# Kernel optimization log

Measured on AMD Instinct MI355X. Metric: run time of the kernel, lower is better.

## Reference

```python
import jax, jax.numpy as jnp
import numpy as np


def _apply_1q_batched(state, gate, q):
    # state: (B,2,2,2,2) complex; gate: (B,2,2) complex; acts on qubit q
    state = jnp.moveaxis(state, q + 1, -1)
    state = jnp.einsum('bij,b...j->b...i', gate, state)
    return jnp.moveaxis(state, -1, q + 1)


def _apply_cnot(state, c, t):
    # flip target bit where control bit == 1
    s0, s1 = jnp.split(state, 2, axis=c + 1)
    s1 = jnp.flip(s1, axis=t + 1)
    return jnp.concatenate([s0, s1], axis=c + 1)


def _quantum_features(angles, params):
    # angles: (B,4) RY rotation angles; params: (4,) RZ angles
    B = angles.shape[0]
    state = jnp.zeros((B, 16), jnp.complex64).at[:, 0].set(1.0).reshape(B, 2, 2, 2, 2)
    # RY(x_i) on each wire (batched angle per sample)
    for q in range(4):
        th = 0.5 * angles[:, q]
        c, s = jnp.cos(th), jnp.sin(th)
        gate = jnp.stack([jnp.stack([c, -s], -1), jnp.stack([s, c], -1)], -2).astype(jnp.complex64)
        state = _apply_1q_batched(state, gate, q)
    # RZ(params[i]) on wire i followed by CNOT(i, (i+1)%4), interleaved as in source
    pc = params.astype(jnp.complex64)
    for q in range(4):
        ph = jnp.exp(jnp.array([-0.5j, 0.5j], jnp.complex64) * pc[q])
        shp = [1, 1, 1, 1, 1]
        shp[q + 1] = 2
        state = state * ph.reshape(shp)
        state = _apply_cnot(state, q, (q + 1) % 4)
    probs = state.real ** 2 + state.imag ** 2  # (B,2,2,2,2)
    feats = []
    for q in range(4):
        axes = tuple(a for a in range(1, 5) if a != q + 1)
        p = probs.sum(axes)  # (B,2)
        feats.append(p[:, 0] - p[:, 1])  # <Z_q>
    return jnp.stack(feats, -1)  # (B,4)


def _deconv2x2(x, w, b):
    # PyTorch ConvTranspose2d with kernel=stride=2, padding=0 (non-overlapping)
    # x: (B,Ci,H,W), w: (Ci,Co,2,2), b: (Co,)
    B, Ci, H, W = x.shape
    Co = w.shape[1]
    y = jnp.einsum('bchw,codk->bohdwk', x, w).reshape(B, Co, 2 * H, 2 * W)
    return y + b[None, :, None, None]


def setup_inputs() -> dict:
    key = jax.random.key(0)
    ks = jax.random.split(key, 10)
    B = 16384
    return {
        'x': jax.random.uniform(ks[0], (B, 1, 28, 28), jnp.float32),
        'var_params': jax.random.normal(ks[1], (4,), jnp.float32),
        'w_lat': jax.random.normal(ks[2], (224, 4), jnp.float32) * 0.3,
        'b_lat': jax.random.normal(ks[3], (224,), jnp.float32) * 0.05,
        'w_fc': jax.random.normal(ks[4], (392, 224), jnp.float32) * 0.05,
        'b_fc': jax.random.normal(ks[5], (392,), jnp.float32) * 0.05,
        'w_d1': jax.random.normal(ks[6], (8, 4, 2, 2), jnp.float32) * 0.2,
        'b_d1': jax.random.normal(ks[7], (4,), jnp.float32) * 0.05,
        'w_d2': jax.random.normal(ks[8], (4, 1, 2, 2), jnp.float32) * 0.2,
        'b_d2': jax.random.normal(ks[9], (1,), jnp.float32) * 0.05,
    }


def reference(x, var_params, w_lat, b_lat, w_fc, b_fc, w_d1, b_d1, w_d2, b_d2):
    # quadrant means -> 4 angles per sample
    quad = jnp.stack([
        x[:, 0, :14, :14].mean((1, 2)),
        x[:, 0, :14, 14:].mean((1, 2)),
        x[:, 0, 14:, :14].mean((1, 2)),
        x[:, 0, 14:, 14:].mean((1, 2)),
    ], axis=1)  # (B,4)
    qf = _quantum_features(quad, var_params)  # (B,4)
    latent = jax.nn.relu(qf @ w_lat.T + b_lat)  # (B,224)
    h = jax.nn.relu(latent @ w_fc.T + b_fc)  # (B,392)
    h = h.reshape(-1, 8, 7, 7)
    h = jax.nn.relu(_deconv2x2(h, w_d1, b_d1))  # (B,4,14,14)
    out = jax.nn.sigmoid(_deconv2x2(h, w_d2, b_d2))  # (B,1,28,28)
    return out
```

## Files before the change

kernel.cpp:

```cpp
#include <hip/hip_runtime.h>
#include <math.h>

#define G 16
#define HS2 400
#define LSTR 232

typedef __attribute__((ext_vector_type(8))) __bf16 bf16x8;
typedef __attribute__((ext_vector_type(4))) float f32x4;
typedef __attribute__((ext_vector_type(2))) float f32x2;

__global__ void wconv_kernel(const float* __restrict__ w_fc, __bf16* __restrict__ wb) {
  int tile = blockIdx.x;
  int kt   = blockIdx.y;
  int lane = threadIdx.x;
  int n  = tile * 16 + (lane & 15);
  int k0 = kt * 32 + (lane >> 4) * 8;
  bf16x8 v;
  if (n < 392) {
    const float* src = w_fc + (size_t)n * 224 + k0;
    float4 f0 = *(const float4*)(src);
    float4 f1 = *(const float4*)(src + 4);
    v[0] = (__bf16)f0.x; v[1] = (__bf16)f0.y; v[2] = (__bf16)f0.z; v[3] = (__bf16)f0.w;
    v[4] = (__bf16)f1.x; v[5] = (__bf16)f1.y; v[6] = (__bf16)f1.z; v[7] = (__bf16)f1.w;
  } else {
    #pragma unroll
    for (int j = 0; j < 8; ++j) v[j] = (__bf16)0.f;
  }
  *(bf16x8*)(wb + ((size_t)(tile * 7 + kt) * 64 + lane) * 8) = v;
}

__global__ __launch_bounds__(512, 8) void fused_kernel(
    const float* __restrict__ x, const float* __restrict__ params,
    const __bf16* __restrict__ wb,
    const float* __restrict__ w_lat, const float* __restrict__ b_lat,
    const float* __restrict__ b_fc,
    const float* __restrict__ w_d1, const float* __restrict__ b_d1,
    const float* __restrict__ w_d2, const float* __restrict__ b_d2,
    float* __restrict__ out, int B)
{
  __shared__ __align__(16) __bf16 latb[G * LSTR];
  __shared__ __align__(16) __bf16 hbuf[G * HS2];
  __shared__ __align__(16) float qfs[G * 4];
  __shared__ float wd1[128];
  __shared__ float wd2[16];
  __shared__ float bd1[4];
  const int t = threadIdx.x;
  const int wv = t >> 6;
  const int lane = t & 63;
  const int s0g = blockIdx.x * G;
  if (s0g >= B) return;

  if (t < 128) wd1[t] = w_d1[t];
  else if (t < 144) wd2[t - 128] = w_d2[t - 128];
  else if (t < 148) bd1[t - 144] = b_d1[t - 144];

  {
    const float* xb = x + (size_t)(s0g + wv * 2) * 784;
    f32x4 vb[2][4];
    #pragma unroll
    for (int smp = 0; smp < 2; ++smp)
      #pragma unroll
      for (int it = 0; it < 4; ++it) {
        int i4 = lane + it * 64;
        if (i4 < 196)
          vb[smp][it] = __builtin_nontemporal_load((const f32x4*)(xb + smp * 784 + i4 * 4));
        else
          vb[smp][it] = (f32x4){0.f, 0.f, 0.f, 0.f};
      }
    float acc[2][4];
    #pragma unroll
    for (int i = 0; i < 2; ++i)
      #pragma unroll
      for (int q = 0; q < 4; ++q) acc[i][q] = 0.f;
    #pragma unroll
    for (int it = 0; it < 4; ++it) {
      int i4 = lane + it * 64;
      int base = i4 * 4;
      int r = base / 28;
      int cb = base - r * 28;
      float bt = (r >= 14) ? 1.f : 0.f;
      float tp = 1.f - bt;
      float w0[4], w1[4], w2[4], w3[4];
      #pragma unroll
      for (int e = 0; e < 4; ++e) {
        float lf = ((cb + e) < 14) ? 1.f : 0.f;
        float rf = 1.f - lf;
        w0[e] = tp * lf; w1[e] = tp * rf; w2[e] = bt * lf; w3[e] = bt * rf;
      }
      #pragma unroll
      for (int smp = 0; smp < 2; ++smp) {
        f32x4 v = vb[smp][it];
        #pragma unroll
        for (int e = 0; e < 4; ++e) {
          acc[smp][0] = fmaf(v[e], w0[e], acc[smp][0]);
          acc[smp][1] = fmaf(v[e], w1[e], acc[smp][1]);
          acc[smp][2] = fmaf(v[e], w2[e], acc[smp][2]);
          acc[smp][3] = fmaf(v[e], w3[e], acc[smp][3]);
        }
      }
    }
    #pragma unroll
    for (int smp = 0; smp < 2; ++smp)
      #pragma unroll
      for (int q = 0; q < 4; ++q)
        #pragma unroll
        for (int o = 32; o > 0; o >>= 1)
          acc[smp][q] += __shfl_down(acc[smp][q], o, 64);
    if (lane == 0) {
      const float inv = 1.f / 196.f;
      #pragma unroll
      for (int smp = 0; smp < 2; ++smp) {
        float4 o;
        o.x = acc[smp][0] * inv; o.y = acc[smp][1] * inv;
        o.z = acc[smp][2] * inv; o.w = acc[smp][3] * inv;
        *(float4*)(qfs + (wv * 2 + smp) * 4) = o;
      }
    }
  }

  {
    const int sub = lane >> 4;
    const int i   = lane & 15;
    const int s   = wv * 2 + (sub & 1);
    float4 mn = *(const float4*)(qfs + s * 4);
    float c_[4], s_[4];
    c_[0] = __cosf(0.5f * mn.x); s_[0] = __sinf(0.5f * mn.x);
    c_[1] = __cosf(0.5f * mn.y); s_[1] = __sinf(0.5f * mn.y);
    c_[2] = __cosf(0.5f * mn.z); s_[2] = __sinf(0.5f * mn.z);
    c_[3] = __cosf(0.5f * mn.w); s_[3] = __sinf(0.5f * mn.w);
    float re = (((i >> 3) & 1) ? s_[0] : c_[0]) * (((i >> 2) & 1) ? s_[1] : c_[1])
             * (((i >> 1) & 1) ? s_[2] : c_[2]) * ((i & 1) ? s_[3] : c_[3]);
    float im = 0.f;
    #pragma unroll
    for (int q = 0; q < 4; ++q) {
      float hp = 0.5f * params[q];
      float sp = __sinf(hp), cp = __cosf(hp);
      int qb = 3 - q;
      float sg = ((i >> qb) & 1) ? sp : -sp;
      float r0 = re, i0 = im;
      re = r0 * cp - i0 * sg;
      im = r0 * sg + i0 * cp;
      int cm = 1 << qb;
      int tm = 1 << (3 - ((q + 1) & 3));
      int srcI = (i & cm) ? (i ^ tm) : i;
      int srcLane = (lane & ~15) | srcI;
      re = __shfl(re, srcLane, 64);
      im = __shfl(im, srcLane, 64);
    }
    float p = re * re + im * im;
    float z[4];
    #pragma unroll
    for (int q = 0; q < 4; ++q) {
      int qb = 3 - q;
      float v = ((i >> qb) & 1) ? -p : p;
      v += __shfl_xor(v, 1, 16);
      v += __shfl_xor(v, 2, 16);
      v += __shfl_xor(v, 4, 16);
      v += __shfl_xor(v, 8, 16);
      z[q] = v;
    }
    if (sub < 2 && i < 4) {
      float zv = (i == 0) ? z[0] : (i == 1) ? z[1] : (i == 2) ? z[2] : z[3];
      qfs[s * 4 + i] = zv;
    }
  }

  #pragma unroll
  for (int sl = 0; sl < 2; ++sl) {
    int s = wv * 2 + sl;
    float4 q4 = *(const float4*)(qfs + s * 4);
    for (int j = lane; j < 224; j += 64) {
      float4 w = *(const float4*)(w_lat + j * 4);
      float a = b_lat[j];
      a = fmaf(q4.x, w.x, a);
      a = fmaf(q4.y, w.y, a);
      a = fmaf(q4.z, w.z, a);
      a = fmaf(q4.w, w.w, a);
      latb[s * LSTR + j] = (__bf16)fmaxf(a, 0.f);
    }
  }
  __syncthreads();

  {
    const int m = lane & 15;
    const int kq = lane >> 4;
    const __bf16* arow = latb + m * LSTR + kq * 8;
    for (int tile = wv; tile < 25; tile += 8) {
      f32x4 acc = {0.f, 0.f, 0.f, 0.f};
      const bf16x8* bp = (const bf16x8*)(wb + ((size_t)(tile * 7) * 64 + lane) * 8);
      #pragma unroll
      for (int kt = 0; kt < 7; ++kt) {
        bf16x8 a = *(const bf16x8*)(arow + kt * 32);
        bf16x8 b = bp[kt * 64];
        acc = __builtin_amdgcn_mfma_f32_16x16x32_bf16(a, b, acc, 0, 0, 0);
      }
      int j = tile * 16 + m;
      if (j < 392) {
        float bf = b_fc[j];
        #pragma unroll
        for (int r = 0; r < 4; ++r)
          hbuf[(kq * 4 + r) * HS2 + j] = (__bf16)fmaxf(acc[r] + bf, 0.f);
      }
    }
  }
  __syncthreads();

  const float bd2v = b_d2[0];
  for (int v = t; v < G * 196; v += 512) {
    int s = v / 196;
    int p = v - s * 196;
    int Y = p / 14;
    int X = p - Y * 14;
    int y = Y >> 1, ey = Y & 1, xx = X >> 1, ex = X & 1;
    const __bf16* hs = hbuf + s * HS2 + y * 7 + xx;
    float hv[8];
    #pragma unroll
    for (int ci = 0; ci < 8; ++ci) hv[ci] = (float)hs[ci * 49];
    float o1[4];
    #pragma unroll
    for (int co = 0; co < 4; ++co) {
      float a = bd1[co];
      #pragma unroll
      for (int ci = 0; ci < 8; ++ci)
        a = fmaf(hv[ci], wd1[ci * 16 + co * 4 + ey * 2 + ex], a);
      o1[co] = fmaxf(a, 0.f);
    }
    size_t basep = (size_t)(s0g + s) * 784;
    #pragma unroll
    for (int dy = 0; dy < 2; ++dy) {
      float v0 = bd2v, v1 = bd2v;
      #pragma unroll
      for (int co = 0; co < 4; ++co) {
        v0 = fmaf(o1[co], wd2[co * 4 + dy * 2 + 0], v0);
        v1 = fmaf(o1[co], wd2[co * 4 + dy * 2 + 1], v1);
      }
      f32x2 o;
      o[0] = 1.f / (1.f + __expf(-v0));
      o[1] = 1.f / (1.f + __expf(-v1));
      __builtin_nontemporal_store(o, (f32x2*)(out + basep + (size_t)(2 * Y + dy) * 28 + 2 * X));
    }
  }
}

extern "C" void kernel_launch(void* const* d_in, const int* in_sizes, int n_in,
                              void* d_out, int out_size, void* d_ws, size_t ws_size,
                              hipStream_t stream) {
  const float* x          = (const float*)d_in[0];
  const float* var_params = (const float*)d_in[1];
  const float* w_lat      = (const float*)d_in[2];
  const float* b_lat      = (const float*)d_in[3];
  const float* w_fc       = (const float*)d_in[4];
  const float* b_fc       = (const float*)d_in[5];
  const float* w_d1       = (const float*)d_in[6];
  const float* b_d1       = (const float*)d_in[7];
  const float* w_d2       = (const float*)d_in[8];
  const float* b_d2       = (const float*)d_in[9];
  float* out = (float*)d_out;

  __bf16* wb = (__bf16*)d_ws;

  int B = in_sizes[0] / 784;
  wconv_kernel<<<dim3(25, 7), 64, 0, stream>>>(w_fc, wb);
  fused_kernel<<<(B + G - 1) / G, 512, 0, stream>>>(
      x, var_params, wb, w_lat, b_lat, b_fc, w_d1, b_d1, w_d2, b_d2, out, B);
}
```

Measured before the change: 135.6 us.

## Process two sample groups per block with prefetch, restructure deconv epilogue layout

Each block now handles two groups of 16 samples and prefetches the second group's input while the first group's quantum and GEMM stages run. The hidden buffer is relaid out channel-interleaved so each deconv thread reads one 16-byte vector and produces a 4x4 output patch written as four float4 nontemporal stores, replacing scattered 8-byte stores. The RZ cos/sin values are computed once in the weight-conversion kernel, and launch bounds are relaxed to 4 blocks per SM. The risks are higher register pressure from the prefetched vectors and half as many blocks for spreading work across the GPU.

```diff
diff --git a/kernel.cpp b/kernel.cpp
--- a/kernel.cpp
+++ b/kernel.cpp
@@ -2,14 +2,14 @@
 #include <math.h>
 
 #define G 16
-#define HS2 400
+#define HS 408
 #define LSTR 232
 
 typedef __attribute__((ext_vector_type(8))) __bf16 bf16x8;
 typedef __attribute__((ext_vector_type(4))) float f32x4;
-typedef __attribute__((ext_vector_type(2))) float f32x2;
-
-__global__ void wconv_kernel(const float* __restrict__ w_fc, __bf16* __restrict__ wb) {
+
+__global__ void wconv_kernel(const float* __restrict__ w_fc, const float* __restrict__ params,
+                             __bf16* __restrict__ wb, float* __restrict__ aux) {
   int tile = blockIdx.x;
   int kt   = blockIdx.y;
   int lane = threadIdx.x;
@@ -27,11 +27,31 @@
     for (int j = 0; j < 8; ++j) v[j] = (__bf16)0.f;
   }
   *(bf16x8*)(wb + ((size_t)(tile * 7 + kt) * 64 + lane) * 8) = v;
+  if (tile == 0 && kt == 0 && lane < 4) {
+    float hp = 0.5f * params[lane];
+    aux[2 * lane]     = __cosf(hp);
+    aux[2 * lane + 1] = __sinf(hp);
+  }
 }
 
-__global__ __launch_bounds__(512, 8) void fused_kernel(
-    const float* __restrict__ x, const float* __restrict__ params,
-    const __bf16* __restrict__ wb,
+__device__ __forceinline__ void load_vb(f32x4 (&dst)[2][4], const float* __restrict__ x,
+                                        int sbase, int wv, int lane) {
+  const float* xb = x + (size_t)(sbase + wv * 2) * 784;
+  #pragma unroll
+  for (int smp = 0; smp < 2; ++smp)
+    #pragma unroll
+    for (int it = 0; it < 4; ++it) {
+      int i4 = lane + it * 64;
+      if (i4 < 196)
+        dst[smp][it] = __builtin_nontemporal_load((const f32x4*)(xb + smp * 784 + i4 * 4));
+      else
+        dst[smp][it] = (f32x4){0.f, 0.f, 0.f, 0.f};
+    }
+}
+
+__global__ __launch_bounds__(512, 4) void fused_kernel(
+    const float* __restrict__ x, const __bf16* __restrict__ wb,
+    const float* __restrict__ aux,
     const float* __restrict__ w_lat, const float* __restrict__ b_lat,
     const float* __restrict__ b_fc,
     const float* __restrict__ w_d1, const float* __restrict__ b_d1,
@@ -39,206 +59,225 @@
     float* __restrict__ out, int B)
 {
   __shared__ __align__(16) __bf16 latb[G * LSTR];
-  __shared__ __align__(16) __bf16 hbuf[G * HS2];
+  __shared__ __align__(16) __bf16 hbuf[G * HS];
   __shared__ __align__(16) float qfs[G * 4];
-  __shared__ float wd1[128];
-  __shared__ float wd2[16];
-  __shared__ float bd1[4];
+  __shared__ __align__(16) float wd1[128];
+  __shared__ __align__(16) float wd2[16];
+  __shared__ __align__(16) float bd1[4];
   const int t = threadIdx.x;
   const int wv = t >> 6;
   const int lane = t & 63;
-  const int s0g = blockIdx.x * G;
-  if (s0g >= B) return;
+  int s0 = blockIdx.x * (2 * G);
+  if (s0 >= B) return;
 
   if (t < 128) wd1[t] = w_d1[t];
   else if (t < 144) wd2[t - 128] = w_d2[t - 128];
   else if (t < 148) bd1[t - 144] = b_d1[t - 144];
 
-  {
-    const float* xb = x + (size_t)(s0g + wv * 2) * 784;
-    f32x4 vb[2][4];
-    #pragma unroll
-    for (int smp = 0; smp < 2; ++smp)
+  f32x4 vb[2][4];
+  load_vb(vb, x, s0, wv, lane);
+
+  #pragma unroll
+  for (int g = 0; g < 2; ++g) {
+    {
+      float acc[2][4];
+      #pragma unroll
+      for (int i = 0; i < 2; ++i)
+        #pragma unroll
+        for (int q = 0; q < 4; ++q) acc[i][q] = 0.f;
       #pragma unroll
       for (int it = 0; it < 4; ++it) {
         int i4 = lane + it * 64;
-        if (i4 < 196)
-          vb[smp][it] = __builtin_nontemporal_load((const f32x4*)(xb + smp * 784 + i4 * 4));
-        else
-          vb[smp][it] = (f32x4){0.f, 0.f, 0.f, 0.f};
-      }
-    float acc[2][4];
+        int base = i4 * 4;
+        int r = base / 28;
+        int cb = base - r * 28;
+        float bt = (r >= 14) ? 1.f : 0.f;
+        float tp = 1.f - bt;
+        float w0[4], w1[4], w2[4], w3[4];
+        #pragma unroll
+        for (int e = 0; e < 4; ++e) {
+          float lf = ((cb + e) < 14) ? 1.f : 0.f;
+          float rf = 1.f - lf;
+          w0[e] = tp * lf; w1[e] = tp * rf; w2[e] = bt * lf; w3[e] = bt * rf;
+        }
+        #pragma unroll
+        for (int smp = 0; smp < 2; ++smp) {
+          f32x4 v = vb[smp][it];
+          #pragma unroll
+          for (int e = 0; e < 4; ++e) {
+            acc[smp][0] = fmaf(v[e], w0[e], acc[smp][0]);
+            acc[smp][1] = fmaf(v[e], w1[e], acc[smp][1]);
+            acc[smp][2] = fmaf(v[e], w2[e], acc[smp][2]);
+            acc[smp][3] = fmaf(v[e], w3[e], acc[smp][3]);
+          }
+        }
+      }
+      #pragma unroll
+      for (int smp = 0; smp < 2; ++smp)
+        #pragma unroll
+        for (int q = 0; q < 4; ++q)
+          #pragma unroll
+          for (int o = 32; o > 0; o >>= 1)
+            acc[smp][q] += __shfl_down(acc[smp][q], o, 64);
+      if (lane == 0) {
+        const float inv = 1.f / 196.f;
+        #pragma unroll
+        for (int smp = 0; smp < 2; ++smp) {
+          float4 o;
+          o.x = acc[smp][0] * inv; o.y = acc[smp][1] * inv;
+          o.z = acc[smp][2] * inv; o.w = acc[smp][3] * inv;
+          *(float4*)(qfs + (wv * 2 + smp) * 4) = o;
+        }
+      }
+    }
+
+    if (g == 0 && s0 + G < B) load_vb(vb, x, s0 + G, wv, lane);
+
+    {
+      const int sub = lane >> 4;
+      const int i   = lane & 15;
+      const int s   = wv * 2 + (sub & 1);
+      float4 mn = *(const float4*)(qfs + s * 4);
+      float c_[4], s_[4];
+      c_[0] = __cosf(0.5f * mn.x); s_[0] = __sinf(0.5f * mn.x);
+      c_[1] = __cosf(0.5f * mn.y); s_[1] = __sinf(0.5f * mn.y);
+      c_[2] = __cosf(0.5f * mn.z); s_[2] = __sinf(0.5f * mn.z);
+      c_[3] = __cosf(0.5f * mn.w); s_[3] = __sinf(0.5f * mn.w);
+      float re = (((i >> 3) & 1) ? s_[0] : c_[0]) * (((i >> 2) & 1) ? s_[1] : c_[1])
+               * (((i >> 1) & 1) ? s_[2] : c_[2]) * ((i & 1) ? s_[3] : c_[3]);
+      float im = 0.f;
+      #pragma unroll
+      for (int q = 0; q < 4; ++q) {
+        float cp = aux[2 * q], sp = aux[2 * q + 1];
+        int qb = 3 - q;
+        float sg = ((i >> qb) & 1) ? sp : -sp;
+        float r0 = re, i0 = im;
+        re = r0 * cp - i0 * sg;
+        im = r0 * sg + i0 * cp;
+        int cm = 1 << qb;
+        int tm = 1 << (3 - ((q + 1) & 3));
+        int srcI = (i & cm) ? (i ^ tm) : i;
+        int srcLane = (lane & ~15) | srcI;
+        re = __shfl(re, srcLane, 64);
+        im = __shfl(im, srcLane, 64);
+      }
+      float p = re * re + im * im;
+      float z[4];
+      #pragma unroll
+      for (int q = 0; q < 4; ++q) {
+        int qb = 3 - q;
+        float v = ((i >> qb) & 1) ? -p : p;
+        v += __shfl_xor(v, 1, 16);
+        v += __shfl_xor(v, 2, 16);
+        v += __shfl_xor(v, 4, 16);
+        v += __shfl_xor(v, 8, 16);
+        z[q] = v;
+      }
+      if (sub < 2 && i < 4) {
+        float zv = (i == 0) ? z[0] : (i == 1) ? z[1] : (i == 2) ? z[2] : z[3];
+        qfs[s * 4 + i] = zv;
+      }
+    }
+
     #pragma unroll
-    for (int i = 0; i < 2; ++i)
-      #pragma unroll
-      for (int q = 0; q < 4; ++q) acc[i][q] = 0.f;
-    #pragma unroll
-    for (int it = 0; it < 4; ++it) {
-      int i4 = lane + it * 64;
-      int base = i4 * 4;
-      int r = base / 28;
-      int cb = base - r * 28;
-      float bt = (r >= 14) ? 1.f : 0.f;
-      float tp = 1.f - bt;
-      float w0[4], w1[4], w2[4], w3[4];
-      #pragma unroll
-      for (int e = 0; e < 4; ++e) {
-        float lf = ((cb + e) < 14) ? 1.f : 0.f;
-        float rf = 1.f - lf;
-        w0[e] = tp * lf; w1[e] = tp * rf; w2[e] = bt * lf; w3[e] = bt * rf;
-      }
-      #pragma unroll
-      for (int smp = 0; smp < 2; ++smp) {
-        f32x4 v = vb[smp][it];
-        #pragma unroll
-        for (int e = 0; e < 4; ++e) {
-          acc[smp][0] = fmaf(v[e], w0[e], acc[smp][0]);
-          acc[smp][1] = fmaf(v[e], w1[e], acc[smp][1]);
-          acc[smp][2] = fmaf(v[e], w2[e], acc[smp][2]);
-          acc[smp][3] = fmaf(v[e], w3[e], acc[smp][3]);
-        }
-      }
-    }
-    #pragma unroll
-    for (int smp = 0; smp < 2; ++smp)
-      #pragma unroll
-      for (int q = 0; q < 4; ++q)
-        #pragma unroll
-        for (int o = 32; o > 0; o >>= 1)
-          acc[smp][q] += __shfl_down(acc[smp][q], o, 64);
-    if (lane == 0) {
-      const float inv = 1.f / 196.f;
-      #pragma unroll
-      for (int smp = 0; smp < 2; ++smp) {
-        float4 o;
-        o.x = acc[smp][0] * inv; o.y = acc[smp][1] * inv;
-        o.z = acc[smp][2] * inv; o.w = acc[smp][3] * inv;
-        *(float4*)(qfs + (wv * 2 + smp) * 4) = o;
-      }
-    }
-  }
-
-  {
-    const int sub = lane >> 4;
-    const int i   = lane & 15;
-    const int s   = wv * 2 + (sub & 1);
-    float4 mn = *(const float4*)(qfs + s * 4);
-    float c_[4], s_[4];
-    c_[0] = __cosf(0.5f * mn.x); s_[0] = __sinf(0.5f * mn.x);
-    c_[1] = __cosf(0.5f * mn.y); s_[1] = __sinf(0.5f * mn.y);
-    c_[2] = __cosf(0.5f * mn.z); s_[2] = __sinf(0.5f * mn.z);
-    c_[3] = __cosf(0.5f * mn.w); s_[3] = __sinf(0.5f * mn.w);
-    float re = (((i >> 3) & 1) ? s_[0] : c_[0]) * (((i >> 2) & 1) ? s_[1] : c_[1])
-             * (((i >> 1) & 1) ? s_[2] : c_[2]) * ((i & 1) ? s_[3] : c_[3]);
-    float im = 0.f;
-    #pragma unroll
-    for (int q = 0; q < 4; ++q) {
-      float hp = 0.5f * params[q];
-      float sp = __sinf(hp), cp = __cosf(hp);
-      int qb = 3 - q;
-      float sg = ((i >> qb) & 1) ? sp : -sp;
-      float r0 = re, i0 = im;
-      re = r0 * cp - i0 * sg;
-      im = r0 * sg + i0 * cp;
-      int cm = 1 << qb;
-      int tm = 1 << (3 - ((q + 1) & 3));
-      int srcI = (i & cm) ? (i ^ tm) : i;
-      int srcLane = (lane & ~15) | srcI;
-      re = __shfl(re, srcLane, 64);
-      im = __shfl(im, srcLane, 64);
-    }
-    float p = re * re + im * im;
-    float z[4];
-    #pragma unroll
-    for (int q = 0; q < 4; ++q) {
-      int qb = 3 - q;
-      float v = ((i >> qb) & 1) ? -p : p;
-      v += __shfl_xor(v, 1, 16);
-      v += __shfl_xor(v, 2, 16);
-      v += __shfl_xor(v, 4, 16);
-      v += __shfl_xor(v, 8, 16);
-      z[q] = v;
-    }
-    if (sub < 2 && i < 4) {
-      float zv = (i == 0) ? z[0] : (i == 1) ? z[1] : (i == 2) ? z[2] : z[3];
-      qfs[s * 4 + i] = zv;
-    }
-  }
-
-  #pragma unroll
-  for (int sl = 0; sl < 2; ++sl) {
-    int s = wv * 2 + sl;
-    float4 q4 = *(const float4*)(qfs + s * 4);
-    for (int j = lane; j < 224; j += 64) {
-      float4 w = *(const float4*)(w_lat + j * 4);
-      float a = b_lat[j];
-      a = fmaf(q4.x, w.x, a);
-      a = fmaf(q4.y, w.y, a);
-      a = fmaf(q4.z, w.z, a);
-      a = fmaf(q4.w, w.w, a);
-      latb[s * LSTR + j] = (__bf16)fmaxf(a, 0.f);
-    }
-  }
-  __syncthreads();
-
-  {
-    const int m = lane & 15;
-    const int kq = lane >> 4;
-    const __bf16* arow = latb + m * LSTR + kq * 8;
-    for (int tile = wv; tile < 25; tile += 8) {
-      f32x4 acc = {0.f, 0.f, 0.f, 0.f};
-      const bf16x8* bp = (const bf16x8*)(wb + ((size_t)(tile * 7) * 64 + lane) * 8);
-      #pragma unroll
-      for (int kt = 0; kt < 7; ++kt) {
-        bf16x8 a = *(const bf16x8*)(arow + kt * 32);
-        bf16x8 b = bp[kt * 64];
-        acc = __builtin_amdgcn_mfma_f32_16x16x32_bf16(a, b, acc, 0, 0, 0);
-      }
-      int j = tile * 16 + m;
-      if (j < 392) {
-        float bf = b_fc[j];
-        #pragma unroll
-        for (int r = 0; r < 4; ++r)
-          hbuf[(kq * 4 + r) * HS2 + j] = (__bf16)fmaxf(acc[r] + bf, 0.f);
-      }
-    }
-  }
-  __syncthreads();
-
-  const float bd2v = b_d2[0];
-  for (int v = t; v < G * 196; v += 512) {
-    int s = v / 196;
-    int p = v - s * 196;
-    int Y = p / 14;
-    int X = p - Y * 14;
-    int y = Y >> 1, ey = Y & 1, xx = X >> 1, ex = X & 1;
-    const __bf16* hs = hbuf + s * HS2 + y * 7 + xx;
-    float hv[8];
-    #pragma unroll
-    for (int ci = 0; ci < 8; ++ci) hv[ci] = (float)hs[ci * 49];
-    float o1[4];
-    #pragma unroll
-    for (int co = 0; co < 4; ++co) {
-      float a = bd1[co];
-      #pragma unroll
-      for (int ci = 0; ci < 8; ++ci)
-        a = fmaf(hv[ci], wd1[ci * 16 + co * 4 + ey * 2 + ex], a);
-      o1[co] = fmaxf(a, 0.f);
-    }
-    size_t basep = (size_t)(s0g + s) * 784;
-    #pragma unroll
-    for (int dy = 0; dy < 2; ++dy) {
-      float v0 = bd2v, v1 = bd2v;
-      #pragma unroll
-      for (int co = 0; co < 4; ++co) {
-        v0 = fmaf(o1[co], wd2[co * 4 + dy * 2 + 0], v0);
-        v1 = fmaf(o1[co], wd2[co * 4 + dy * 2 + 1], v1);
-      }
-      f32x2 o;
-      o[0] = 1.f / (1.f + __expf(-v0));
-      o[1] = 1.f / (1.f + __expf(-v1));
-      __builtin_nontemporal_store(o, (f32x2*)(out + basep + (size_t)(2 * Y + dy) * 28 + 2 * X));
-    }
+    for (int sl = 0; sl < 2; ++sl) {
+      int s = wv * 2 + sl;
+      float4 q4 = *(const float4*)(qfs + s * 4);
+      for (int j = lane; j < 224; j += 64) {
+        float4 w = *(const float4*)(w_lat + j * 4);
+        float a = b_lat[j];
+        a = fmaf(q4.x, w.x, a);
+        a = fmaf(q4.y, w.y, a);
+        a = fmaf(q4.z, w.z, a);
+        a = fmaf(q4.w, w.w, a);
+        latb[s * LSTR + j] = (__bf16)fmaxf(a, 0.f);
+      }
+    }
+    __syncthreads();
+
+    {
+      const int m = lane & 15;
+      const int kq = lane >> 4;
+      const __bf16* arow = latb + m * LSTR + kq * 8;
+      for (int tile = wv; tile < 25; tile += 8) {
+        f32x4 acc = {0.f, 0.f, 0.f, 0.f};
+        const bf16x8* bp = (const bf16x8*)(wb + ((size_t)(tile * 7) * 64 + lane) * 8);
+        #pragma unroll
+        for (int kt = 0; kt < 7; ++kt) {
+          bf16x8 a = *(const bf16x8*)(arow + kt * 32);
+          bf16x8 b = bp[kt * 64];
+          acc = __builtin_amdgcn_mfma_f32_16x16x32_bf16(a, b, acc, 0, 0, 0);
+        }
+        int j = tile * 16 + m;
+        if (j < 392) {
+          float bf = b_fc[j];
+          int ci = j / 49;
+          int off = (j - ci * 49) * 8 + ci;
+          #pragma unroll
+          for (int r = 0; r < 4; ++r)
+            hbuf[(kq * 4 + r) * HS + off] = (__bf16)fmaxf(acc[r] + bf, 0.f);
+        }
+      }
+    }
+    __syncthreads();
+
+    {
+      const float bd2v = b_d2[0];
+      f32x4 w2v[4];
+      #pragma unroll
+      for (int co = 0; co < 4; ++co) w2v[co] = *(const f32x4*)(wd2 + co * 4);
+      f32x4 b1v = *(const f32x4*)(bd1);
+      for (int v = t; v < G * 49; v += 512) {
+        int s = v / 49;
+        int pos = v - s * 49;
+        int y = pos / 7;
+        int xx = pos - y * 7;
+        bf16x8 hb = *(const bf16x8*)(hbuf + s * HS + pos * 8);
+        f32x4 o1q[4];
+        #pragma unroll
+        for (int co = 0; co < 4; ++co)
+          o1q[co] = (f32x4){b1v[co], b1v[co], b1v[co], b1v[co]};
+        #pragma unroll
+        for (int ci = 0; ci < 8; ++ci) {
+          float h = (float)hb[ci];
+          #pragma unroll
+          for (int co = 0; co < 4; ++co) {
+            f32x4 w1 = *(const f32x4*)(wd1 + ci * 16 + co * 4);
+            #pragma unroll
+            for (int p = 0; p < 4; ++p) o1q[co][p] = fmaf(h, w1[p], o1q[co][p]);
+          }
+        }
+        #pragma unroll
+        for (int co = 0; co < 4; ++co)
+          #pragma unroll
+          for (int p = 0; p < 4; ++p) o1q[co][p] = fmaxf(o1q[co][p], 0.f);
+        f32x4 q4[4];
+        #pragma unroll
+        for (int p4 = 0; p4 < 4; ++p4) {
+          f32x4 a2 = (f32x4){bd2v, bd2v, bd2v, bd2v};
+          #pragma unroll
+          for (int co = 0; co < 4; ++co) {
+            float o = o1q[co][p4];
+            #pragma unroll
+            for (int d = 0; d < 4; ++d) a2[d] = fmaf(o, w2v[co][d], a2[d]);
+          }
+          #pragma unroll
+          for (int d = 0; d < 4; ++d) a2[d] = 1.f / (1.f + __expf(-a2[d]));
+          q4[p4] = a2;
+        }
+        f32x4 r0 = {q4[0][0], q4[0][1], q4[1][0], q4[1][1]};
+        f32x4 r1 = {q4[0][2], q4[0][3], q4[1][2], q4[1][3]};
+        f32x4 r2 = {q4[2][0], q4[2][1], q4[3][0], q4[3][1]};
+        f32x4 r3 = {q4[2][2], q4[2][3], q4[3][2], q4[3][3]};
+        float* ob = out + (size_t)(s0 + s) * 784 + (size_t)(4 * y) * 28 + 4 * xx;
+        __builtin_nontemporal_store(r0, (f32x4*)(ob));
+        __builtin_nontemporal_store(r1, (f32x4*)(ob + 28));
+        __builtin_nontemporal_store(r2, (f32x4*)(ob + 56));
+        __builtin_nontemporal_store(r3, (f32x4*)(ob + 84));
+      }
+    }
+    s0 += G;
+    if (s0 >= B) break;
   }
 }
 
@@ -258,9 +297,10 @@
   float* out = (float*)d_out;
 
   __bf16* wb = (__bf16*)d_ws;
+  float* aux = (float*)((char*)d_ws + (size_t)25 * 7 * 64 * 8 * sizeof(__bf16));
 
   int B = in_sizes[0] / 784;
-  wconv_kernel<<<dim3(25, 7), 64, 0, stream>>>(w_fc, wb);
-  fused_kernel<<<(B + G - 1) / G, 512, 0, stream>>>(
-      x, var_params, wb, w_lat, b_lat, b_fc, w_d1, b_d1, w_d2, b_d2, out, B);
+  wconv_kernel<<<dim3(25, 7), 64, 0, stream>>>(w_fc, var_params, wb, aux);
+  fused_kernel<<<(B + 2 * G - 1) / (2 * G), 512, 0, stream>>>(
+      x, wb, aux, w_lat, b_lat, b_fc, w_d1, b_d1, w_d2, b_d2, out, B);
 }
```

After: 208.5 us. +53.8%, slower.
